# Kernel optimization log

Measured on AMD Instinct MI355X. Metric: run time of the kernel, lower is better.

The kernel has to match this reference:

```python
import jax, jax.numpy as jnp
import numpy as np

DIM = 2048
H = 16
DK = 128
DV = 128
KCONV = 4
EPS = 1e-6
B = 2
S = 2048
KD = H * DK  # 2048
VD = H * DV  # 2048


def setup_inputs() -> dict:
    key = jax.random.key(0)
    ks = jax.random.split(key, 16)
    sc = 0.02
    inp = {
        "x": jax.random.normal(ks[0], (B, S, DIM), dtype=jnp.float32),
        "Wq": jax.random.normal(ks[1], (KD, DIM), dtype=jnp.float32) * sc,
        "Wk": jax.random.normal(ks[2], (KD, DIM), dtype=jnp.float32) * sc,
        "Wv": jax.random.normal(ks[3], (VD, DIM), dtype=jnp.float32) * sc,
        "Wa": jax.random.normal(ks[4], (H, DIM), dtype=jnp.float32) * sc,
        "Wb": jax.random.normal(ks[5], (H, DIM), dtype=jnp.float32) * sc,
        "Wg": jax.random.normal(ks[6], (VD, DIM), dtype=jnp.float32) * sc,
        "Wo": jax.random.normal(ks[7], (DIM, VD), dtype=jnp.float32) * sc,
        "cw_q": jax.random.normal(ks[8], (KD, KCONV), dtype=jnp.float32) * 0.3,
        "cb_q": jnp.zeros((KD,), dtype=jnp.float32),
        "cw_k": jax.random.normal(ks[9], (KD, KCONV), dtype=jnp.float32) * 0.3,
        "cb_k": jnp.zeros((KD,), dtype=jnp.float32),
        "cw_v": jax.random.normal(ks[10], (VD, KCONV), dtype=jnp.float32) * 0.3,
        "cb_v": jnp.zeros((VD,), dtype=jnp.float32),
        "A_log": jnp.zeros((H,), dtype=jnp.float32),
        "dt_bias": jnp.zeros((H,), dtype=jnp.float32),
        "norm_w": jnp.ones((VD,), dtype=jnp.float32),
    }
    return inp


def _causal_conv(x, w, b):
    # x: [B, S, C]; w: [C, K]; b: [C]. Depthwise causal conv (zero init state) + SiLU.
    Bb, Ss, C = x.shape
    xp = jnp.pad(x, ((0, 0), (KCONV - 1, 0), (0, 0)))
    out = b
    for j in range(KCONV):
        out = out + xp[:, j:j + Ss, :] * w[:, j]
    return jax.nn.silu(out)


def _l2norm(x):
    n = jnp.sqrt(jnp.sum(x * x, axis=-1, keepdims=True))
    return x / jnp.maximum(n, 1e-12)


def _forward(x, Wq, Wk, Wv, Wa, Wb, Wg, Wo, cw_q, cb_q, cw_k, cb_k, cw_v, cb_v,
             A_log, dt_bias, norm_w):
    Bb, Ss, _ = x.shape
    q = _causal_conv(x @ Wq.T, cw_q, cb_q)  # [B,S,KD]
    k = _causal_conv(x @ Wk.T, cw_k, cb_k)
    v = _causal_conv(x @ Wv.T, cw_v, cb_v)

    a = x @ Wa.T  # [B,S,H]
    b = x @ Wb.T
    g = jnp.exp(-jnp.exp(A_log)[None, None, :] * jax.nn.softplus(a + dt_bias[None, None, :]))
    beta = jax.nn.sigmoid(b)

    q = _l2norm(q.reshape(Bb, Ss, H, DK))
    k = _l2norm(k.reshape(Bb, Ss, H, DK))
    v = v.reshape(Bb, Ss, H, DV)

    S0 = jnp.zeros((Bb, H, DK, DV), dtype=x.dtype)

    def step(Sstate, inputs):
        q_t, k_t, v_t, g_t, beta_t = inputs  # [B,H,DK],[B,H,DK],[B,H,DV],[B,H],[B,H]
        retrieved = jnp.einsum('bhkv,bhk->bhv', Sstate, k_t)
        error = v_t - g_t[..., None] * retrieved
        update = k_t[..., :, None] * (beta_t[..., None] * error)[..., None, :]
        Snew = g_t[..., None, None] * Sstate + update
        o_t = jnp.einsum('bhkv,bhk->bhv', Snew, q_t)
        return Snew, o_t

    # scan over time: move time axis to front
    xs = (q.transpose(1, 0, 2, 3), k.transpose(1, 0, 2, 3), v.transpose(1, 0, 2, 3),
          g.transpose(1, 0, 2), beta.transpose(1, 0, 2))
    _, o = jax.lax.scan(step, S0, xs)  # o: [S,B,H,DV]
    o = o.transpose(1, 0, 2, 3).reshape(Bb, Ss, VD)

    # RMSNorm
    o = o * jax.lax.rsqrt(jnp.mean(o * o, axis=-1, keepdims=True) + EPS) * norm_w
    o = o * jax.nn.silu(x @ Wg.T)
    return o @ Wo.T


def reference(x, Wq, Wk, Wv, Wa, Wb, Wg, Wo, cw_q, cb_q, cw_k, cb_k, cw_v, cb_v,
              A_log, dt_bias, norm_w):
    return _forward(x, Wq, Wk, Wv, Wa, Wb, Wg, Wo, cw_q, cb_q, cw_k, cb_k,
                    cw_v, cb_v, A_log, dt_bias, norm_w)
```

## Files before the change

### kernel.cpp

```cpp
#include <hip/hip_runtime.h>

#define S_LEN   2048
#define NH      16
#define DIM     2048
#define KD      2048
#define VD      2048
#define MB      1048576ull
#define CT      64
#define NC      32

typedef short  short8  __attribute__((ext_vector_type(8)));
typedef short  short4v __attribute__((ext_vector_type(4)));
typedef float  floatx4 __attribute__((ext_vector_type(4)));

#define MFMA(a, b, c) __builtin_amdgcn_mfma_f32_16x16x32_bf16((a), (b), (c), 0, 0, 0)

__device__ inline short f2bf(float x) {
    unsigned u = __float_as_uint(x);
    unsigned r = (u + 0x7fffu + ((u >> 16) & 1u)) >> 16;
    return (short)r;
}
__device__ inline float bf2f(short s) {
    return __uint_as_float(((unsigned)(unsigned short)s) << 16);
}
__device__ inline float silu_f(float x) { return x / (1.f + __expf(-x)); }

__device__ inline short8 neg8(short8 a) {
    unsigned* p = (unsigned*)&a;
    p[0] ^= 0x80008000u; p[1] ^= 0x80008000u;
    p[2] ^= 0x80008000u; p[3] ^= 0x80008000u;
    return a;
}

__device__ inline void load_lds16(const void* g, void* l) {
    __builtin_amdgcn_global_load_lds(
        (const __attribute__((address_space(1))) unsigned int*)g,
        (__attribute__((address_space(3))) unsigned int*)l, 16, 0, 0);
}

__global__ __launch_bounds__(256) void cvt_all_kernel(
    const float* __restrict__ x,  const float* __restrict__ Wq,
    const float* __restrict__ Wk, const float* __restrict__ Wv,
    const float* __restrict__ Wg, const float* __restrict__ Wo,
    short* __restrict__ xb,  short* __restrict__ Wqb, short* __restrict__ Wkb,
    short* __restrict__ Wvb, short* __restrict__ Wgb, short* __restrict__ Wob) {
    const float* in; short* out; int n8;
    switch (blockIdx.y) {
        case 0:  in = x;  out = xb;  n8 = 1048576; break;
        case 1:  in = Wq; out = Wqb; n8 = 524288;  break;
        case 2:  in = Wk; out = Wkb; n8 = 524288;  break;
        case 3:  in = Wv; out = Wvb; n8 = 524288;  break;
        case 4:  in = Wg; out = Wgb; n8 = 524288;  break;
        default: in = Wo; out = Wob; n8 = 524288;  break;
    }
    int i = blockIdx.x * 256 + threadIdx.x;
    if (i >= n8) return;
    float4 a = ((const float4*)in)[2 * i];
    float4 b = ((const float4*)in)[2 * i + 1];
    short8 o;
    o[0] = f2bf(a.x); o[1] = f2bf(a.y); o[2] = f2bf(a.z); o[3] = f2bf(a.w);
    o[4] = f2bf(b.x); o[5] = f2bf(b.y); o[6] = f2bf(b.z); o[7] = f2bf(b.w);
    ((short8*)out)[i] = o;
}

__device__ inline void store_c(float* C, size_t idx, float v) { C[idx] = v; }
__device__ inline void store_c(short* C, size_t idx, float v) { C[idx] = f2bf(v); }

template <typename OutT>
__device__ inline void gemm_tile(const short* __restrict__ A, const short* __restrict__ Bw,
                                 OutT* __restrict__ C, int mtile, int ntile) {
    __shared__ short lA[128 * 32];
    __shared__ short lB[128 * 32];
    const int K = 2048, N = 2048;
    int t    = threadIdx.x;
    int wave = t >> 6;
    int lane = t & 63;
    int m0 = mtile * 128, n0 = ntile * 128;
    int wm = (wave & 1) * 64;
    int wn = (wave >> 1) * 64;

    floatx4 acc[4][4];
#pragma unroll
    for (int i = 0; i < 4; ++i)
#pragma unroll
        for (int j = 0; j < 4; ++j) acc[i][j] = (floatx4){0.f, 0.f, 0.f, 0.f};

    int fr = lane & 15;
    int fk = (lane >> 4) * 8;

    for (int k0 = 0; k0 < K; k0 += 32) {
#pragma unroll
        for (int p = 0; p < 2; ++p) {
            int c   = p * 256 + t;
            int row = c >> 2, kp = c & 3;
            const short* ga = A  + (size_t)(m0 + row) * K + k0 + kp * 8;
            const short* gb = Bw + (size_t)(n0 + row) * K + k0 + kp * 8;
            short* la = lA + (size_t)(p * 256 + wave * 64) * 8;
            short* lb = lB + (size_t)(p * 256 + wave * 64) * 8;
            load_lds16(ga, la);
            load_lds16(gb, lb);
        }
        __syncthreads();
        short8 af[4], bfr[4];
#pragma unroll
        for (int i = 0; i < 4; ++i) af[i]  = *(const short8*)(lA + (wm + i * 16 + fr) * 32 + fk);
#pragma unroll
        for (int j = 0; j < 4; ++j) bfr[j] = *(const short8*)(lB + (wn + j * 16 + fr) * 32 + fk);
#pragma unroll
        for (int i = 0; i < 4; ++i)
#pragma unroll
            for (int j = 0; j < 4; ++j)
                acc[i][j] = MFMA(af[i], bfr[j], acc[i][j]);
        __syncthreads();
    }
    int cr = (lane >> 4) * 4;
    int cc = lane & 15;
#pragma unroll
    for (int i = 0; i < 4; ++i)
#pragma unroll
        for (int j = 0; j < 4; ++j)
#pragma unroll
            for (int r = 0; r < 4; ++r)
                store_c(C, (size_t)(m0 + wm + i * 16 + cr + r) * N + (n0 + wn + j * 16 + cc),
                        acc[i][j][r]);
}

__global__ __launch_bounds__(256) void gemm_out(const short* __restrict__ A,
    const short* __restrict__ Bw, float* __restrict__ C) {
    gemm_tile<float>(A, Bw, C, blockIdx.x, blockIdx.y);
}


#define VM(n_) asm volatile("s_waitcnt vmcnt(" #n_ ")" ::: "memory");

#define STAGE8(s_, isB_)                                                     \
    {                                                                        \
        const char* gsrc = (isB_) ? (const char*)Bw : (const char*)A;        \
        int t0 = (isB_) ? n0 : m0;                                           \
        char* dbase = smem + ((s_) & 3) * 32768 + (isB_) * 16384;            \
        _Pragma("unroll")                                                    \
        for (int ld = 0; ld < 2; ++ld) {                                     \
            int ch = ld * 8 + wave;                                          \
            int Pl = (ch << 10) + (lane << 4);                               \
            int Q  = Pl ^ (((lane >> 2) & 3) << 4);                          \
            const char* src = gsrc + ((size_t)(t0 + (Q >> 6)) << 12)         \
                              + ((size_t)(s_) << 6) + (Q & 63);              \
            load_lds16(src, dbase + (ch << 10));                             \
        }                                                                    \
    }

#define PHASE8(s_, qm_, LOADB_, STG, WAIT)                                   \
    {                                                                        \
        const char* sb = smem + ((s_) & 3) * 32768;                          \
        short8 af[4];                                                        \
        if (LOADB_) {                                                        \
            _Pragma("unroll")                                                \
            for (int nf = 0; nf < 4; ++nf)                                   \
                bfr[nf] = *(const short8*)(sb + 16384 +                      \
                    ((rowB_base + nf * 16) << 6) + qsw);                     \
        }                                                                    \
        _Pragma("unroll")                                                    \
        for (int mf = 0; mf < 4; ++mf)                                       \
            af[mf] = *(const short8*)(sb +                                   \
                ((rowA_base + (qm_) * 64 + mf * 16) << 6) + qsw);            \
        STG                                                                  \
        __builtin_amdgcn_s_barrier();                                        \
        asm volatile("s_waitcnt lgkmcnt(0)" ::: "memory");                   \
        __builtin_amdgcn_s_setprio(1);                                       \
        _Pragma("unroll")                                                    \
        for (int mf = 0; mf < 4; ++mf)                                       \
            _Pragma("unroll")                                                \
            for (int nf = 0; nf < 4; ++nf)                                   \
                acc[(qm_) * 4 + mf][nf] =                                    \
                    MFMA(af[mf], bfr[nf], acc[(qm_) * 4 + mf][nf]);          \
        __builtin_amdgcn_s_setprio(0);                                       \
        WAIT                                                                 \
        __builtin_amdgcn_s_barrier();                                        \
    }

__global__ __launch_bounds__(512) void gemm8_qkvg(const short* __restrict__ A,
    const short* __restrict__ B0, const short* __restrict__ B1,
    const short* __restrict__ B2, const short* __restrict__ B3,
    short* __restrict__ C0, short* __restrict__ C1,
    short* __restrict__ C2, short* __restrict__ C3) {
    extern __shared__ char smem[];
    const short* Bw; short* C;
    switch (blockIdx.z) {
        case 0:  Bw = B0; C = C0; break;
        case 1:  Bw = B1; C = C1; break;
        case 2:  Bw = B2; C = C2; break;
        default: Bw = B3; C = C3; break;
    }
    int x  = blockIdx.x;
    int xs = (x & 7) * 16 + (x >> 3);
    int m0 = (xs >> 3) * 256;
    int n0 = (xs & 7) * 256;
    int tid  = threadIdx.x;
    int wave = tid >> 6, lane = tid & 63;
    int l16  = lane & 15, quad = lane >> 4;
    int wm = wave >> 2, wn = wave & 3;
    int qsw = ((quad ^ (l16 & 3)) << 4);
    int rowA_base = wm * 128 + l16;
    int rowB_base = wn * 64 + l16;

    floatx4 acc[8][4];
#pragma unroll
    for (int i = 0; i < 8; ++i)
#pragma unroll
        for (int j = 0; j < 4; ++j) acc[i][j] = (floatx4){0.f, 0.f, 0.f, 0.f};
    short8 bfr[4];

    STAGE8(0, 0) STAGE8(0, 1)
    STAGE8(1, 0) STAGE8(1, 1)
    STAGE8(2, 0) STAGE8(2, 1)
    VM(8)
    __builtin_amdgcn_s_barrier();

#pragma unroll 1
    for (int T = 0; T < 30; ++T) {
        int s0 = 2 * T, s1 = 2 * T + 1, sa = 2 * T + 3, sb2 = 2 * T + 4;
        PHASE8(s0, 0, 1, STAGE8(sa, 0), )
        PHASE8(s0, 1, 0, STAGE8(sa, 1), VM(8))
        PHASE8(s1, 0, 1, STAGE8(sb2, 0), )
        PHASE8(s1, 1, 0, STAGE8(sb2, 1), VM(8))
    }
    PHASE8(60, 0, 1, STAGE8(63, 0), )
    PHASE8(60, 1, 0, STAGE8(63, 1), VM(8))
    PHASE8(61, 0, 1, , )
    PHASE8(61, 1, 0, , VM(4))
    PHASE8(62, 0, 1, , )
    PHASE8(62, 1, 0, , VM(0))
    PHASE8(63, 0, 1, , )
    PHASE8(63, 1, 0, , )

#pragma unroll
    for (int i = 0; i < 8; ++i) {
        int row0 = m0 + wm * 128 + (i >> 2) * 64 + (i & 3) * 16 + quad * 4;
#pragma unroll
        for (int nf = 0; nf < 4; ++nf) {
            int col = n0 + wn * 64 + nf * 16 + l16;
#pragma unroll
            for (int r = 0; r < 4; ++r)
                C[(size_t)(row0 + r) * 2048 + col] = f2bf(acc[i][nf][r]);
        }
    }
}

__global__ __launch_bounds__(256) void ab_kernel(const float* __restrict__ x,
    const float* __restrict__ Wa, const float* __restrict__ Wb,
    const float* __restrict__ Alog, const float* __restrict__ dtb,
    float* __restrict__ gdec, float* __restrict__ beta) {
    __shared__ float xs[2048];
    __shared__ float red[32][9];
    int m = blockIdx.x, t = threadIdx.x;
    const float* xr = x + (size_t)m * DIM;
    for (int i = t; i < 512; i += 256) ((float4*)xs)[i] = ((const float4*)xr)[i];
    __syncthreads();
    int col = t >> 3, part = t & 7;
    const float* wr = (col < 16) ? (Wa + (size_t)col * DIM) : (Wb + (size_t)(col - 16) * DIM);
    float s = 0.f;
    int kb = part * 256;
#pragma unroll 4
    for (int k = 0; k < 256; k += 4) {
        float4 xv = *(const float4*)(xs + kb + k);
        float4 wv = *(const float4*)(wr + kb + k);
        s += xv.x * wv.x + xv.y * wv.y + xv.z * wv.z + xv.w * wv.w;
    }
    red[col][part] = s;
    __syncthreads();
    if (t < 32) {
        float a = 0.f;
#pragma unroll
        for (int p = 0; p < 8; ++p) a += red[t][p];
        if (t < 16) {
            float sp = a + dtb[t];
            float softp = (sp > 20.f) ? sp : log1pf(expf(sp));
            gdec[(size_t)m * NH + t] = expf(-expf(Alog[t]) * softp);
        } else {
            int h = t - 16;
            beta[(size_t)m * NH + h] = 1.f / (1.f + expf(-a));
        }
    }
}

__global__ __launch_bounds__(256) void conv_kernel(
    const short* __restrict__ qr, const short* __restrict__ kr, const short* __restrict__ vr,
    const float* __restrict__ cwq, const float* __restrict__ cbq,
    const float* __restrict__ cwk, const float* __restrict__ cbk,
    const float* __restrict__ cwv, const float* __restrict__ cbv,
    short* __restrict__ qn, short* __restrict__ kn, short* __restrict__ vc) {
    int gw   = blockIdx.x * 4 + (threadIdx.x >> 6);
    int lane = threadIdx.x & 63;
    int h  = gw & (NH - 1);
    int m  = gw >> 4;
    int tt = m & (S_LEN - 1);
    int c  = h * 128 + lane * 2;
    size_t rowbase = (size_t)m * KD + c;

    float4 wq0 = ((const float4*)cwq)[c], wq1 = ((const float4*)cwq)[c + 1];
    float4 wk0 = ((const float4*)cwk)[c], wk1 = ((const float4*)cwk)[c + 1];
    float4 wv0 = ((const float4*)cwv)[c], wv1 = ((const float4*)cwv)[c + 1];
    float q0 = cbq[c], q1 = cbq[c + 1];
    float k0 = cbk[c], k1 = cbk[c + 1];
    float v0 = cbv[c], v1 = cbv[c + 1];
    const float* wq0a = (const float*)&wq0; const float* wq1a = (const float*)&wq1;
    const float* wk0a = (const float*)&wk0; const float* wk1a = (const float*)&wk1;
    const float* wv0a = (const float*)&wv0; const float* wv1a = (const float*)&wv1;
#pragma unroll
    for (int j = 0; j < 4; ++j) {
        int ts = tt - 3 + j;
        if (ts >= 0) {
            long long rb = (long long)rowbase + (long long)(j - 3) * KD;
            unsigned uq = *(const unsigned*)(qr + rb);
            unsigned uk = *(const unsigned*)(kr + rb);
            unsigned uv = *(const unsigned*)(vr + rb);
            q0 += bf2f((short)(uq & 0xffff)) * wq0a[j]; q1 += bf2f((short)(uq >> 16)) * wq1a[j];
            k0 += bf2f((short)(uk & 0xffff)) * wk0a[j]; k1 += bf2f((short)(uk >> 16)) * wk1a[j];
            v0 += bf2f((short)(uv & 0xffff)) * wv0a[j]; v1 += bf2f((short)(uv >> 16)) * wv1a[j];
        }
    }
    q0 = silu_f(q0); q1 = silu_f(q1);
    k0 = silu_f(k0); k1 = silu_f(k1);
    v0 = silu_f(v0); v1 = silu_f(v1);

    float sq = q0 * q0 + q1 * q1;
    float sk = k0 * k0 + k1 * k1;
#pragma unroll
    for (int off = 1; off < 64; off <<= 1) {
        sq += __shfl_xor(sq, off);
        sk += __shfl_xor(sk, off);
    }
    float iq = 1.f / fmaxf(sqrtf(sq), 1e-12f);
    float ik = 1.f / fmaxf(sqrtf(sk), 1e-12f);
    unsigned oq = (unsigned)(unsigned short)f2bf(q0 * iq) | ((unsigned)(unsigned short)f2bf(q1 * iq) << 16);
    unsigned ok = (unsigned)(unsigned short)f2bf(k0 * ik) | ((unsigned)(unsigned short)f2bf(k1 * ik) << 16);
    unsigned ov = (unsigned)(unsigned short)f2bf(v0)      | ((unsigned)(unsigned short)f2bf(v1)      << 16);
    *(unsigned*)(qn + rowbase) = oq;
    *(unsigned*)(kn + rowbase) = ok;
    *(unsigned*)(vc + rowbase) = ov;
}

__global__ __launch_bounds__(256) void solve_kernel(
    const short* __restrict__ kn, const short* __restrict__ vn,
    const float* __restrict__ gdec, const float* __restrict__ beta,
    short* __restrict__ UvT, short* __restrict__ Tk) {
    __shared__ short Pn[64][72];
    __shared__ short Pt[64][72];
    __shared__ short UT[128][72];
    __shared__ float Ls[64];
    __shared__ float Bs[64];

    int wg   = blockIdx.x;
    int half = wg & 1;
    int c    = (wg >> 1) & 31;
    int bh   = wg >> 6;
    int b = bh >> 4, h = bh & 15;
    int tid = threadIdx.x;
    int wave = tid >> 6, lane = tid & 63;
    int quad = lane >> 4, l16 = lane & 15;

    const short* Kb = kn + ((size_t)(b * S_LEN + c * CT)) * KD + h * 128;
    const short* Vb = vn + ((size_t)(b * S_LEN + c * CT)) * KD + h * 128;

    if (wave == 0) {
        float lg = __logf(gdec[((size_t)(b * S_LEN + c * CT) + lane) * NH + h]);
#pragma unroll
        for (int off = 1; off < 64; off <<= 1) {
            float y = __shfl_up(lg, off);
            if (lane >= off) lg += y;
        }
        Ls[lane] = lg;
        Bs[lane] = beta[((size_t)(b * S_LEN + c * CT) + lane) * NH + h];
    }
    __syncthreads();

    {
        floatx4 acc[4];
#pragma unroll
        for (int i = 0; i < 4; ++i) acc[i] = (floatx4){0.f, 0.f, 0.f, 0.f};
        for (int ks = 0; ks < 4; ++ks) {
            short8 af = *(const short8*)(Kb + (size_t)(wave * 16 + l16) * KD + ks * 32 + quad * 8);
#pragma unroll
            for (int it = 0; it < 4; ++it) {
                short8 bf = *(const short8*)(Kb + (size_t)(it * 16 + l16) * KD + ks * 32 + quad * 8);
                acc[it] = MFMA(af, bf, acc[it]);
            }
        }
#pragma unroll
        for (int it = 0; it < 4; ++it) {
            int icol = it * 16 + l16;
#pragma unroll
            for (int r = 0; r < 4; ++r) {
                int trow = wave * 16 + quad * 4 + r;
                float v = 0.f;
                if (icol < trow) v = -Bs[trow] * __expf(Ls[trow] - Ls[icol]) * acc[it][r];
                short bv = f2bf(v);
                Pn[trow][icol] = bv;
                Pt[icol][trow] = bv;
            }
        }
    }

    {
        const short* src = half ? Kb : Vb;
        int tr = tid >> 2, seg = (tid & 3) * 32;
        float s = Bs[tr] * (half ? __expf(Ls[tr]) : 1.f);
#pragma unroll
        for (int j = 0; j < 4; ++j) {
            short8 d = *(const short8*)(src + (size_t)tr * KD + seg + j * 8);
#pragma unroll
            for (int e = 0; e < 8; ++e)
                UT[seg + j * 8 + e][tr] = f2bf(bf2f(d[e]) * s);
        }
    }
    __syncthreads();

    for (int iter = 0; iter < 6; ++iter) {
        floatx4 acc[8];
#pragma unroll
        for (int nt = 0; nt < 8; ++nt) {
            short4v u4 = *(const short4v*)&UT[nt * 16 + l16][wave * 16 + quad * 4];
            floatx4 a;
#pragma unroll
            for (int e = 0; e < 4; ++e) a[e] = bf2f(u4[e]);
            acc[nt] = a;
        }
        for (int ks = 0; ks < 2; ++ks) {
            short8 af = *(const short8*)&Pn[wave * 16 + l16][ks * 32 + quad * 8];
#pragma unroll
            for (int nt = 0; nt < 8; ++nt) {
                short8 bf = *(const short8*)&UT[nt * 16 + l16][ks * 32 + quad * 8];
                acc[nt] = MFMA(af, bf, acc[nt]);
            }
        }
        __syncthreads();
        if (iter < 5) {
#pragma unroll
            for (int nt = 0; nt < 8; ++nt) {
                short4v w4;
#pragma unroll
                for (int e = 0; e < 4; ++e) w4[e] = f2bf(acc[nt][e]);
                *(short4v*)&UT[nt * 16 + l16][wave * 16 + quad * 4] = w4;
            }
            floatx4 pacc[4];
#pragma unroll
            for (int it = 0; it < 4; ++it) pacc[it] = (floatx4){0.f, 0.f, 0.f, 0.f};
            for (int ks = 0; ks < 2; ++ks) {
                short8 paf = *(const short8*)&Pn[wave * 16 + l16][ks * 32 + quad * 8];
#pragma unroll
                for (int it = 0; it < 4; ++it) {
                    short8 pbf = *(const short8*)&Pt[it * 16 + l16][ks * 32 + quad * 8];
                    pacc[it] = MFMA(paf, pbf, pacc[it]);
                }
            }
            __syncthreads();
#pragma unroll
            for (int it = 0; it < 4; ++it) {
                int icol = it * 16 + l16;
#pragma unroll
                for (int r = 0; r < 4; ++r) {
                    int trow = wave * 16 + quad * 4 + r;
                    short bv = f2bf(pacc[it][r]);
                    Pn[trow][icol] = bv;
                    Pt[icol][trow] = bv;
                }
            }
            __syncthreads();
        } else {
            size_t cb = (size_t)(bh * NC + c);
            if (half == 0) {
#pragma unroll
                for (int nt = 0; nt < 8; ++nt) {
                    short4v w4;
#pragma unroll
                    for (int e = 0; e < 4; ++e) w4[e] = f2bf(acc[nt][e]);
                    *(short4v*)(UvT + (cb * 128 + nt * 16 + l16) * 64 + wave * 16 + quad * 4) = w4;
                }
            } else {
#pragma unroll
                for (int nt = 0; nt < 8; ++nt)
#pragma unroll
                    for (int r = 0; r < 4; ++r)
                        Tk[(cb * 64 + wave * 16 + quad * 4 + r) * 128 + nt * 16 + l16] = f2bf(acc[nt][r]);
            }
        }
    }
}

__global__ __launch_bounds__(256) void prepb_kernel(
    const short* __restrict__ qn, const short* __restrict__ kn,
    const float* __restrict__ gdec,
    short* __restrict__ Wb_, short* __restrict__ Qg,
    short* __restrict__ KtT, float* __restrict__ gam63) {
    __shared__ short KT[128][72];
    __shared__ float Ls[64];
    int wg = blockIdx.x;
    int c = wg & 31, bh = wg >> 5;
    int b = bh >> 4, h = bh & 15;
    int tid = threadIdx.x, wave = tid >> 6, lane = tid & 63;
    int quad = lane >> 4, l16 = lane & 15;
    const short* Qb = qn + ((size_t)(b * S_LEN + c * CT)) * KD + h * 128;
    const short* Kb = kn + ((size_t)(b * S_LEN + c * CT)) * KD + h * 128;

    if (wave == 0) {
        float lg = __logf(gdec[((size_t)(b * S_LEN + c * CT) + lane) * NH + h]);
#pragma unroll
        for (int off = 1; off < 64; off <<= 1) {
            float y = __shfl_up(lg, off);
            if (lane >= off) lg += y;
        }
        Ls[lane] = lg;
    }
    __syncthreads();
    size_t cb = (size_t)(bh * NC + c);
    if (tid == 0) gam63[cb] = __expf(Ls[63]);

    {
        floatx4 acc[4];
#pragma unroll
        for (int i = 0; i < 4; ++i) acc[i] = (floatx4){0.f, 0.f, 0.f, 0.f};
        for (int ks = 0; ks < 4; ++ks) {
            short8 af = *(const short8*)(Qb + (size_t)(wave * 16 + l16) * KD + ks * 32 + quad * 8);
#pragma unroll
            for (int it = 0; it < 4; ++it) {
                short8 bf = *(const short8*)(Kb + (size_t)(it * 16 + l16) * KD + ks * 32 + quad * 8);
                acc[it] = MFMA(af, bf, acc[it]);
            }
        }
#pragma unroll
        for (int it = 0; it < 4; ++it) {
            int icol = it * 16 + l16;
#pragma unroll
            for (int r = 0; r < 4; ++r) {
                int trow = wave * 16 + quad * 4 + r;
                float v = (icol <= trow) ? __expf(Ls[trow] - Ls[icol]) * acc[it][r] : 0.f;
                Wb_[(cb * 64 + trow) * 64 + icol] = f2bf(v);
            }
        }
    }

    {
        int tr = tid >> 2, seg = (tid & 3) * 32;
        float sq = __expf(Ls[tr]);
        float sk = __expf(Ls[63] - Ls[tr]);
#pragma unroll
        for (int j = 0; j < 4; ++j) {
            short8 dq = *(const short8*)(Qb + (size_t)tr * KD + seg + j * 8);
            short8 dk = *(const short8*)(Kb + (size_t)tr * KD + seg + j * 8);
            short8 oq;
#pragma unroll
            for (int e = 0; e < 8; ++e) {
                oq[e] = f2bf(bf2f(dq[e]) * sq);
                KT[seg + j * 8 + e][tr] = f2bf(bf2f(dk[e]) * sk);
            }
            *(short8*)(Qg + (cb * 64 + tr) * 128 + seg + j * 8) = oq;
        }
    }
    __syncthreads();
    {
        int dk = tid >> 1, seg = (tid & 1) * 32;
#pragma unroll
        for (int j = 0; j < 4; ++j) {
            short8 v = *(const short8*)&KT[dk][seg + j * 8];
            *(short8*)(KtT + (cb * 128 + dk) * 64 + seg + j * 8) = v;
        }
    }
}

__global__ __launch_bounds__(256, 1) void seq_kernel(
    const short* __restrict__ UvT, const short* __restrict__ Tk,
    const short* __restrict__ Wb_, const short* __restrict__ Qg,
    const short* __restrict__ KtT, const float* __restrict__ gam63,
    short* __restrict__ ob) {
    __shared__ short ST[64][136];
    __shared__ short UTs[64][72];
    int wg = blockIdx.x;
    int vh = wg & 1, bh = wg >> 1;
    int b = bh >> 4, h = bh & 15;
    int tid = threadIdx.x, wave = tid >> 6, lane = tid & 63;
    int quad = lane >> 4, l16 = lane & 15;

    for (int i = tid; i < 64 * 136; i += 256) ((short*)ST)[i] = 0;
    floatx4 sacc[8];
#pragma unroll
    for (int i = 0; i < 8; ++i) sacc[i] = (floatx4){0.f, 0.f, 0.f, 0.f};
    __syncthreads();

    short8 tkA[4], qgA[4], wA[2], ktA[16]; short4v uvA[4]; float gamA;
    short8 tkB[4], qgB[4], wB[2], ktB[16]; short4v uvB[4]; float gamB;

#define LOADF(tkX, qgX, wX, ktX, uvX, gamX, c)                                              \
    {                                                                                       \
        size_t cb = (size_t)(bh * NC + (c));                                                \
        const short* Tkc = Tk  + cb * 64 * 128;                                             \
        const short* Qgc = Qg  + cb * 64 * 128;                                             \
        const short* Wc  = Wb_ + cb * 64 * 64;                                              \
        const short* Ktc = KtT + cb * 128 * 64;                                             \
        const short* Uvc = UvT + (cb * 128 + (size_t)vh * 64) * 64;                         \
        _Pragma("unroll")                                                                   \
        for (int ks = 0; ks < 4; ++ks) {                                                    \
            tkX[ks] = *(const short8*)(Tkc + (size_t)(wave * 16 + l16) * 128 + ks * 32 + quad * 8); \
            qgX[ks] = *(const short8*)(Qgc + (size_t)(wave * 16 + l16) * 128 + ks * 32 + quad * 8); \
        }                                                                                   \
        _Pragma("unroll")                                                                   \
        for (int ks = 0; ks < 2; ++ks)                                                      \
            wX[ks] = *(const short8*)(Wc + (size_t)(wave * 16 + l16) * 64 + ks * 32 + quad * 8); \
        _Pragma("unroll")                                                                   \
        for (int dt = 0; dt < 8; ++dt)                                                      \
            _Pragma("unroll")                                                               \
            for (int ks = 0; ks < 2; ++ks)                                                  \
                ktX[dt * 2 + ks] = *(const short8*)(Ktc + (size_t)(dt * 16 + l16) * 64 + ks * 32 + quad * 8); \
        _Pragma("unroll")                                                                   \
        for (int vt = 0; vt < 4; ++vt)                                                      \
            uvX[vt] = *(const short4v*)(Uvc + (size_t)(vt * 16 + l16) * 64 + wave * 16 + quad * 4); \
        gamX = gam63[cb];                                                                   \
    }

#define BODY(tkX, qgX, wX, ktX, uvX, gamX, c)                                               \
    {                                                                                       \
        floatx4 uacc[4], oacc[4];                                                           \
        _Pragma("unroll")                                                                   \
        for (int vt = 0; vt < 4; ++vt) {                                                    \
            floatx4 a;                                                                      \
            _Pragma("unroll")                                                               \
            for (int e = 0; e < 4; ++e) a[e] = bf2f(uvX[vt][e]);                            \
            uacc[vt] = a;                                                                   \
            oacc[vt] = (floatx4){0.f, 0.f, 0.f, 0.f};                                       \
        }                                                                                   \
        _Pragma("unroll")                                                                   \
        for (int ks = 0; ks < 4; ++ks) {                                                    \
            short8 afT = neg8(tkX[ks]);                                                     \
            _Pragma("unroll")                                                               \
            for (int vt = 0; vt < 4; ++vt) {                                                \
                short8 bf = *(const short8*)&ST[vt * 16 + l16][ks * 32 + quad * 8];         \
                uacc[vt] = MFMA(afT, bf, uacc[vt]);                                         \
                oacc[vt] = MFMA(qgX[ks], bf, oacc[vt]);                                     \
            }                                                                               \
        }                                                                                   \
        _Pragma("unroll")                                                                   \
        for (int vt = 0; vt < 4; ++vt) {                                                    \
            short4v w4;                                                                     \
            _Pragma("unroll")                                                               \
            for (int e = 0; e < 4; ++e) w4[e] = f2bf(uacc[vt][e]);                          \
            *(short4v*)&UTs[vt * 16 + l16][wave * 16 + quad * 4] = w4;                      \
        }                                                                                   \
        __syncthreads();                                                                    \
        _Pragma("unroll")                                                                   \
        for (int ks = 0; ks < 2; ++ks) {                                                    \
            _Pragma("unroll")                                                               \
            for (int vt = 0; vt < 4; ++vt) {                                                \
                short8 bf = *(const short8*)&UTs[vt * 16 + l16][ks * 32 + quad * 8];        \
                oacc[vt] = MFMA(wX[ks], bf, oacc[vt]);                                      \
            }                                                                               \
        }                                                                                   \
        _Pragma("unroll")                                                                   \
        for (int vt = 0; vt < 4; ++vt)                                                      \
            _Pragma("unroll")                                                               \
            for (int r = 0; r < 4; ++r) {                                                   \
                int m = b * S_LEN + (c) * CT + wave * 16 + quad * 4 + r;                    \
                ob[(size_t)m * VD + h * 128 + vh * 64 + vt * 16 + l16] = f2bf(oacc[vt][r]); \
            }                                                                               \
        _Pragma("unroll")                                                                   \
        for (int dt = 0; dt < 8; ++dt)                                                      \
            _Pragma("unroll")                                                               \
            for (int e = 0; e < 4; ++e) sacc[dt][e] *= gamX;                                \
        _Pragma("unroll")                                                                   \
        for (int ks = 0; ks < 2; ++ks) {                                                    \
            short8 af = *(const short8*)&UTs[wave * 16 + l16][ks * 32 + quad * 8];          \
            _Pragma("unroll")                                                               \
            for (int dt = 0; dt < 8; ++dt)                                                  \
                sacc[dt] = MFMA(af, ktX[dt * 2 + ks], sacc[dt]);                            \
        }                                                                                   \
        _Pragma("unroll")                                                                   \
        for (int dt = 0; dt < 8; ++dt)                                                      \
            _Pragma("unroll")                                                               \
            for (int r = 0; r < 4; ++r)                                                     \
                ST[wave * 16 + quad * 4 + r][dt * 16 + l16] = f2bf(sacc[dt][r]);            \
        __syncthreads();                                                                    \
    }

    LOADF(tkA, qgA, wA, ktA, uvA, gamA, 0)
    for (int c = 0; c < NC; c += 2) {
        LOADF(tkB, qgB, wB, ktB, uvB, gamB, c + 1)
        BODY(tkA, qgA, wA, ktA, uvA, gamA, c)
        if (c + 2 < NC) LOADF(tkA, qgA, wA, ktA, uvA, gamA, c + 2)
        BODY(tkB, qgB, wB, ktB, uvB, gamB, c + 1)
    }
#undef LOADF
#undef BODY
}

__global__ __launch_bounds__(256) void rms_gate_kernel(
    const short* __restrict__ o, const short* __restrict__ graw,
    const float* __restrict__ nw, short* __restrict__ og) {
    __shared__ float red[4];
    int m = blockIdx.x, t = threadIdx.x;
    short8 a = ((const short8*)(o + (size_t)m * VD))[t];
    float av[8];
#pragma unroll
    for (int i = 0; i < 8; ++i) av[i] = bf2f(a[i]);
    float ss = 0.f;
#pragma unroll
    for (int i = 0; i < 8; ++i) ss += av[i] * av[i];
#pragma unroll
    for (int off = 1; off < 64; off <<= 1) ss += __shfl_xor(ss, off);
    if ((t & 63) == 0) red[t >> 6] = ss;
    __syncthreads();
    float tot = red[0] + red[1] + red[2] + red[3];
    float sc = rsqrtf(tot * (1.f / VD) + 1e-6f);
    short8 gv = ((const short8*)(graw + (size_t)m * VD))[t];
    float4 n0 = ((const float4*)nw)[2 * t];
    float4 n1 = ((const float4*)nw)[2 * t + 1];
    const float* na = (const float*)&n0;
    const float* nb = (const float*)&n1;
    short8 ov;
#pragma unroll
    for (int i = 0; i < 4; ++i) ov[i]     = f2bf(av[i]     * sc * na[i] * silu_f(bf2f(gv[i])));
#pragma unroll
    for (int i = 0; i < 4; ++i) ov[i + 4] = f2bf(av[i + 4] * sc * nb[i] * silu_f(bf2f(gv[i + 4])));
    ((short8*)(og + (size_t)m * VD))[t] = ov;
}

extern "C" void kernel_launch(void* const* d_in, const int* in_sizes, int n_in,
                              void* d_out, int out_size, void* d_ws, size_t ws_size,
                              hipStream_t stream) {
    const float* x    = (const float*)d_in[0];
    const float* Wq   = (const float*)d_in[1];
    const float* Wk   = (const float*)d_in[2];
    const float* Wv   = (const float*)d_in[3];
    const float* Wa   = (const float*)d_in[4];
    const float* Wb   = (const float*)d_in[5];
    const float* Wg   = (const float*)d_in[6];
    const float* Wo   = (const float*)d_in[7];
    const float* cwq  = (const float*)d_in[8];
    const float* cbq  = (const float*)d_in[9];
    const float* cwk  = (const float*)d_in[10];
    const float* cbk  = (const float*)d_in[11];
    const float* cwv  = (const float*)d_in[12];
    const float* cbv  = (const float*)d_in[13];
    const float* Alog = (const float*)d_in[14];
    const float* dtb  = (const float*)d_in[15];
    const float* nw   = (const float*)d_in[16];

    char* ws = (char*)d_ws;
    short* Wob = (short*)(ws);
    short* xb  = (short*)(ws + 8 * MB);
    short* Wqb = (short*)(ws + 24 * MB);
    short* Wkb = (short*)(ws + 32 * MB);
    short* Wvb = (short*)(ws + 40 * MB);
    short* Wgb = (short*)(ws + 48 * MB);
    short* qrb = (short*)(ws + 56 * MB);
    short* krb = (short*)(ws + 72 * MB);
    short* vrb = (short*)(ws + 88 * MB);
    short* grb = (short*)(ws + 104 * MB);
    short* qnb = (short*)(ws + 8 * MB);
    short* knb = (short*)(ws + 24 * MB);
    short* vnb = (short*)(ws + 40 * MB);
    float* gdec = (float*)(ws + 120 * MB);
    float* beta = (float*)(ws + 120 * MB + 262144);
    short* ob  = qrb;
    short* ogb = krb;
    short* UvT  = (short*)(ws + 121 * MB);
    short* Tkb  = (short*)(ws + 137 * MB);
    short* Wbuf = (short*)(ws + 153 * MB);
    short* Qgb  = (short*)(ws + 161 * MB);
    short* KtT  = (short*)(ws + 177 * MB);
    float* gm63 = (float*)(ws + 193 * MB);

    static bool attr_done = false;
    if (!attr_done) {
        hipFuncSetAttribute((const void*)gemm8_qkvg,
                            hipFuncAttributeMaxDynamicSharedMemorySize, 131072);
        attr_done = true;
    }

    cvt_all_kernel<<<dim3(4096, 6), 256, 0, stream>>>(x, Wq, Wk, Wv, Wg, Wo,
                                                      xb, Wqb, Wkb, Wvb, Wgb, Wob);

    ab_kernel<<<4096, 256, 0, stream>>>(x, Wa, Wb, Alog, dtb, gdec, beta);

    gemm8_qkvg<<<dim3(128, 1, 4), 512, 131072, stream>>>(xb, Wqb, Wkb, Wvb, Wgb,
                                                         qrb, krb, vrb, grb);

    conv_kernel<<<16384, 256, 0, stream>>>(qrb, krb, vrb,
                                           cwq, cbq, cwk, cbk, cwv, cbv, qnb, knb, vnb);

    solve_kernel<<<2048, 256, 0, stream>>>(knb, vnb, gdec, beta, UvT, Tkb);
    prepb_kernel<<<1024, 256, 0, stream>>>(qnb, knb, gdec, Wbuf, Qgb, KtT, gm63);
    seq_kernel<<<64, 256, 0, stream>>>(UvT, Tkb, Wbuf, Qgb, KtT, gm63, ob);

    rms_gate_kernel<<<4096, 256, 0, stream>>>(ob, grb, nw, ogb);

    gemm_out<<<dim3(32, 16, 1), 256, 0, stream>>>(ogb, Wob, (float*)d_out);
}
```

Before: 775.2 us.

## Reuse pipelined 256x256 GEMM for output projection and fix LDS swizzle

Turns the multi-stage pipelined 256x256 bf16 GEMM body into a templated tile function. The output projection now uses it instead of the simple 128x128 GEMM with a single synchronous stage. The LDS XOR swizzle pattern is also changed, both on the staging side and in the fragment read offsets, to cut bank conflicts. The output GEMM now launches only 128 blocks of 512 threads with 128KB shared memory, so it trades occupancy for deeper data reuse and load/compute overlap.

```diff
diff --git a/kernel.cpp b/kernel.cpp
--- a/kernel.cpp
+++ b/kernel.cpp
@@ -37,6 +37,9 @@
         (const __attribute__((address_space(1))) unsigned int*)g,
         (__attribute__((address_space(3))) unsigned int*)l, 16, 0, 0);
 }
+
+__device__ inline void store_c(float* C, size_t idx, float v) { C[idx] = v; }
+__device__ inline void store_c(short* C, size_t idx, float v) { C[idx] = f2bf(v); }
 
 __global__ __launch_bounds__(256) void cvt_all_kernel(
     const float* __restrict__ x,  const float* __restrict__ Wq,
@@ -63,73 +66,6 @@
     ((short8*)out)[i] = o;
 }
 
-__device__ inline void store_c(float* C, size_t idx, float v) { C[idx] = v; }
-__device__ inline void store_c(short* C, size_t idx, float v) { C[idx] = f2bf(v); }
-
-template <typename OutT>
-__device__ inline void gemm_tile(const short* __restrict__ A, const short* __restrict__ Bw,
-                                 OutT* __restrict__ C, int mtile, int ntile) {
-    __shared__ short lA[128 * 32];
-    __shared__ short lB[128 * 32];
-    const int K = 2048, N = 2048;
-    int t    = threadIdx.x;
-    int wave = t >> 6;
-    int lane = t & 63;
-    int m0 = mtile * 128, n0 = ntile * 128;
-    int wm = (wave & 1) * 64;
-    int wn = (wave >> 1) * 64;
-
-    floatx4 acc[4][4];
-#pragma unroll
-    for (int i = 0; i < 4; ++i)
-#pragma unroll
-        for (int j = 0; j < 4; ++j) acc[i][j] = (floatx4){0.f, 0.f, 0.f, 0.f};
-
-    int fr = lane & 15;
-    int fk = (lane >> 4) * 8;
-
-    for (int k0 = 0; k0 < K; k0 += 32) {
-#pragma unroll
-        for (int p = 0; p < 2; ++p) {
-            int c   = p * 256 + t;
-            int row = c >> 2, kp = c & 3;
-            const short* ga = A  + (size_t)(m0 + row) * K + k0 + kp * 8;
-            const short* gb = Bw + (size_t)(n0 + row) * K + k0 + kp * 8;
-            short* la = lA + (size_t)(p * 256 + wave * 64) * 8;
-            short* lb = lB + (size_t)(p * 256 + wave * 64) * 8;
-            load_lds16(ga, la);
-            load_lds16(gb, lb);
-        }
-        __syncthreads();
-        short8 af[4], bfr[4];
-#pragma unroll
-        for (int i = 0; i < 4; ++i) af[i]  = *(const short8*)(lA + (wm + i * 16 + fr) * 32 + fk);
-#pragma unroll
-        for (int j = 0; j < 4; ++j) bfr[j] = *(const short8*)(lB + (wn + j * 16 + fr) * 32 + fk);
-#pragma unroll
-        for (int i = 0; i < 4; ++i)
-#pragma unroll
-            for (int j = 0; j < 4; ++j)
-                acc[i][j] = MFMA(af[i], bfr[j], acc[i][j]);
-        __syncthreads();
-    }
-    int cr = (lane >> 4) * 4;
-    int cc = lane & 15;
-#pragma unroll
-    for (int i = 0; i < 4; ++i)
-#pragma unroll
-        for (int j = 0; j < 4; ++j)
-#pragma unroll
-            for (int r = 0; r < 4; ++r)
-                store_c(C, (size_t)(m0 + wm + i * 16 + cr + r) * N + (n0 + wn + j * 16 + cc),
-                        acc[i][j][r]);
-}
-
-__global__ __launch_bounds__(256) void gemm_out(const short* __restrict__ A,
-    const short* __restrict__ Bw, float* __restrict__ C) {
-    gemm_tile<float>(A, Bw, C, blockIdx.x, blockIdx.y);
-}
-
 
 #define VM(n_) asm volatile("s_waitcnt vmcnt(" #n_ ")" ::: "memory");
 
@@ -142,7 +78,7 @@
         for (int ld = 0; ld < 2; ++ld) {                                     \
             int ch = ld * 8 + wave;                                          \
             int Pl = (ch << 10) + (lane << 4);                               \
-            int Q  = Pl ^ (((lane >> 2) & 3) << 4);                          \
+            int Q  = Pl ^ (((lane >> 3) & 3) << 4);                          \
             const char* src = gsrc + ((size_t)(t0 + (Q >> 6)) << 12)         \
                               + ((size_t)(s_) << 6) + (Q & 63);              \
             load_lds16(src, dbase + (ch << 10));                             \
@@ -178,6 +114,65 @@
         __builtin_amdgcn_s_barrier();                                        \
     }
 
+template <typename OutT>
+__device__ __forceinline__ void gemm8_tile(const short* __restrict__ A,
+                                           const short* __restrict__ Bw,
+                                           OutT* __restrict__ C, char* smem) {
+    int x  = blockIdx.x;
+    int xs = (x & 7) * 16 + (x >> 3);
+    int m0 = (xs >> 3) * 256;
+    int n0 = (xs & 7) * 256;
+    int tid  = threadIdx.x;
+    int wave = tid >> 6, lane = tid & 63;
+    int l16  = lane & 15, quad = lane >> 4;
+    int wm = wave >> 2, wn = wave & 3;
+    int qsw = ((quad ^ ((l16 >> 1) & 3)) << 4);
+    int rowA_base = wm * 128 + l16;
+    int rowB_base = wn * 64 + l16;
+
+    floatx4 acc[8][4];
+#pragma unroll
+    for (int i = 0; i < 8; ++i)
+#pragma unroll
+        for (int j = 0; j < 4; ++j) acc[i][j] = (floatx4){0.f, 0.f, 0.f, 0.f};
+    short8 bfr[4];
+
+    STAGE8(0, 0) STAGE8(0, 1)
+    STAGE8(1, 0) STAGE8(1, 1)
+    STAGE8(2, 0) STAGE8(2, 1)
+    VM(8)
+    __builtin_amdgcn_s_barrier();
+
+#pragma unroll 1
+    for (int T = 0; T < 30; ++T) {
+        int s0 = 2 * T, s1 = 2 * T + 1, sa = 2 * T + 3, sb2 = 2 * T + 4;
+        PHASE8(s0, 0, 1, STAGE8(sa, 0), )
+        PHASE8(s0, 1, 0, STAGE8(sa, 1), VM(8))
+        PHASE8(s1, 0, 1, STAGE8(sb2, 0), )
+        PHASE8(s1, 1, 0, STAGE8(sb2, 1), VM(8))
+    }
+    PHASE8(60, 0, 1, STAGE8(63, 0), )
+    PHASE8(60, 1, 0, STAGE8(63, 1), VM(8))
+    PHASE8(61, 0, 1, , )
+    PHASE8(61, 1, 0, , VM(4))
+    PHASE8(62, 0, 1, , )
+    PHASE8(62, 1, 0, , VM(0))
+    PHASE8(63, 0, 1, , )
+    PHASE8(63, 1, 0, , )
+
+#pragma unroll
+    for (int i = 0; i < 8; ++i) {
+        int row0 = m0 + wm * 128 + (i >> 2) * 64 + (i & 3) * 16 + quad * 4;
+#pragma unroll
+        for (int nf = 0; nf < 4; ++nf) {
+            int col = n0 + wn * 64 + nf * 16 + l16;
+#pragma unroll
+            for (int r = 0; r < 4; ++r)
+                store_c(C, (size_t)(row0 + r) * 2048 + col, acc[i][nf][r]);
+        }
+    }
+}
+
 __global__ __launch_bounds__(512) void gemm8_qkvg(const short* __restrict__ A,
     const short* __restrict__ B0, const short* __restrict__ B1,
     const short* __restrict__ B2, const short* __restrict__ B3,
@@ -191,59 +186,13 @@
         case 2:  Bw = B2; C = C2; break;
         default: Bw = B3; C = C3; break;
     }
-    int x  = blockIdx.x;
-    int xs = (x & 7) * 16 + (x >> 3);
-    int m0 = (xs >> 3) * 256;
-    int n0 = (xs & 7) * 256;
-    int tid  = threadIdx.x;
-    int wave = tid >> 6, lane = tid & 63;
-    int l16  = lane & 15, quad = lane >> 4;
-    int wm = wave >> 2, wn = wave & 3;
-    int qsw = ((quad ^ (l16 & 3)) << 4);
-    int rowA_base = wm * 128 + l16;
-    int rowB_base = wn * 64 + l16;
-
-    floatx4 acc[8][4];
-#pragma unroll
-    for (int i = 0; i < 8; ++i)
-#pragma unroll
-        for (int j = 0; j < 4; ++j) acc[i][j] = (floatx4){0.f, 0.f, 0.f, 0.f};
-    short8 bfr[4];
-
-    STAGE8(0, 0) STAGE8(0, 1)
-    STAGE8(1, 0) STAGE8(1, 1)
-    STAGE8(2, 0) STAGE8(2, 1)
-    VM(8)
-    __builtin_amdgcn_s_barrier();
-
-#pragma unroll 1
-    for (int T = 0; T < 30; ++T) {
-        int s0 = 2 * T, s1 = 2 * T + 1, sa = 2 * T + 3, sb2 = 2 * T + 4;
-        PHASE8(s0, 0, 1, STAGE8(sa, 0), )
-        PHASE8(s0, 1, 0, STAGE8(sa, 1), VM(8))
-        PHASE8(s1, 0, 1, STAGE8(sb2, 0), )
-        PHASE8(s1, 1, 0, STAGE8(sb2, 1), VM(8))
-    }
-    PHASE8(60, 0, 1, STAGE8(63, 0), )
-    PHASE8(60, 1, 0, STAGE8(63, 1), VM(8))
-    PHASE8(61, 0, 1, , )
-    PHASE8(61, 1, 0, , VM(4))
-    PHASE8(62, 0, 1, , )
-    PHASE8(62, 1, 0, , VM(0))
-    PHASE8(63, 0, 1, , )
-    PHASE8(63, 1, 0, , )
-
-#pragma unroll
-    for (int i = 0; i < 8; ++i) {
-        int row0 = m0 + wm * 128 + (i >> 2) * 64 + (i & 3) * 16 + quad * 4;
-#pragma unroll
-        for (int nf = 0; nf < 4; ++nf) {
-            int col = n0 + wn * 64 + nf * 16 + l16;
-#pragma unroll
-            for (int r = 0; r < 4; ++r)
-                C[(size_t)(row0 + r) * 2048 + col] = f2bf(acc[i][nf][r]);
-        }
-    }
+    gemm8_tile<short>(A, Bw, C, smem);
+}
+
+__global__ __launch_bounds__(512) void gemm8_out(const short* __restrict__ A,
+    const short* __restrict__ Bw, float* __restrict__ C) {
+    extern __shared__ char smem[];
+    gemm8_tile<float>(A, Bw, C, smem);
 }
 
 __global__ __launch_bounds__(256) void ab_kernel(const float* __restrict__ x,
@@ -771,6 +720,8 @@
     if (!attr_done) {
         hipFuncSetAttribute((const void*)gemm8_qkvg,
                             hipFuncAttributeMaxDynamicSharedMemorySize, 131072);
+        hipFuncSetAttribute((const void*)gemm8_out,
+                            hipFuncAttributeMaxDynamicSharedMemorySize, 131072);
         attr_done = true;
     }
 
@@ -791,5 +742,5 @@
 
     rms_gate_kernel<<<4096, 256, 0, stream>>>(ob, grb, nw, ogb);
 
-    gemm_out<<<dim3(32, 16, 1), 256, 0, stream>>>(ogb, Wob, (float*)d_out);
-}
+    gemm8_out<<<dim3(128, 1, 1), 512, 131072, stream>>>(ogb, Wob, (float*)d_out);
+}
```

Result: faster. 749.0 us (-3.4%).
